# Optimization experiments

Measured on AMD Instinct MI355X. Metric: run time of the kernel, lower is better.

## Reference

```python
import jax, jax.numpy as jnp
import numpy as np

DIM = 512
HIDDEN = DIM * 4


def _act_quant(x):
    # per-token int8 absmax quant over last axis (BitNet b1.58)
    scale = 127.0 / jnp.clip(jnp.max(jnp.abs(x), axis=-1, keepdims=True), 1e-5)
    return jnp.clip(jnp.round(x * scale), -128.0, 127.0) / scale


def _weight_quant(w):
    # ternary {-1,0,1} quant with global mean-abs scale
    scale = 1.0 / jnp.clip(jnp.mean(jnp.abs(w)), 1e-5)
    return jnp.clip(jnp.round(w * scale), -1.0, 1.0) / scale


def _bitlinear(x, w, b):
    # straight-through estimator: forward uses quantized values
    xq = x + jax.lax.stop_gradient(_act_quant(x) - x)
    wq = w + jax.lax.stop_gradient(_weight_quant(w) - w)
    return jnp.einsum('btd,hd->bth', xq, wq) + b


def setup_inputs() -> dict:
    key = jax.random.key(0)
    k1, k2, k3 = jax.random.split(key, 3)
    x = jax.random.normal(k1, (8, 8192, DIM), dtype=jnp.float32)
    w1 = jax.random.normal(k2, (HIDDEN, DIM), dtype=jnp.float32) * (DIM ** -0.5)
    b1 = jnp.zeros((HIDDEN,), dtype=jnp.float32)
    w2 = jax.random.normal(k3, (DIM, HIDDEN), dtype=jnp.float32) * (HIDDEN ** -0.5)
    b2 = jnp.zeros((DIM,), dtype=jnp.float32)
    return {"x": x, "w1": w1, "b1": b1, "w2": w2, "b2": b2}


def reference(x, w1, b1, w2, b2):
    h = _bitlinear(x, w1, b1)                      # [B,T,HIDDEN]
    h = jax.nn.gelu(h, approximate=False)          # exact erf GELU (nn.GELU default)
    return x + _bitlinear(h, w2, b2)               # residual
```

## Files before the change

kernel.cpp:

```cpp
#include <hip/hip_runtime.h>
#include <hip/hip_bf16.h>

#define DIM 512
#define HID 2048
#define MT  64
#define KS1 8
#define KS2 32

typedef __attribute__((ext_vector_type(4))) int      i32x4;
typedef __attribute__((ext_vector_type(4))) unsigned u32x4;
typedef __attribute__((ext_vector_type(2))) unsigned u32x2;
typedef __attribute__((ext_vector_type(2))) __fp16   fp16x2;

#define ASET(ag, v) asm volatile("v_accvgpr_write_b32 %0, %1" : "=a"(ag) : "v"(v))
#define AGET(v, ag) asm volatile("v_accvgpr_read_b32 %0, %1" : "=v"(v) : "a"(ag))

static __device__ __forceinline__ float gelu_erf(float h) {
  const float u  = h * 0.70710678118654752f;
  const float au = fabsf(u);
  const float t  = __builtin_amdgcn_rcpf(fmaf(0.3275911f, au, 1.f));
  float p = fmaf(1.061405429f, t, -1.453152027f);
  p = fmaf(p, t, 1.421413741f);
  p = fmaf(p, t, -0.284496736f);
  p = fmaf(p, t, 0.254829592f);
  p *= t;
  const float e  = __builtin_amdgcn_exp2f(-u * u * 1.4426950408889634f);
  const float ea = fmaf(-p, e, 1.f);
  const float er = __builtin_copysignf(ea, u);
  return fmaf(0.5f * h, er, 0.5f * h);
}

static __device__ __forceinline__ int qi8(float g, float s) {
  return (int)fminf(fmaxf(rintf(g * s), -128.f), 127.f);
}

static __device__ __forceinline__ unsigned q4pack(float4 v, float scl) {
  int q0 = qi8(v.x, scl), q1 = qi8(v.y, scl), q2 = qi8(v.z, scl), q3 = qi8(v.w, scl);
  return (unsigned)(q0 & 255) | ((unsigned)(q1 & 255) << 8) |
         ((unsigned)(q2 & 255) << 16) | ((unsigned)(q3 & 255) << 24);
}

static __device__ __forceinline__ unsigned packf16(float a, float b) {
  fp16x2 v = __builtin_amdgcn_cvt_pkrtz(a, b);
  unsigned u; __builtin_memcpy(&u, &v, 4); return u;
}
static __device__ __forceinline__ float unpackf16(unsigned u, int hi) {
  unsigned short s = (unsigned short)(hi ? (u >> 16) : (u & 0xffff));
  __fp16 h; __builtin_memcpy(&h, &s, 2);
  return (float)h;
}

__global__ void k_wabs(const float* __restrict__ w1, const float* __restrict__ w2,
                       float* __restrict__ part) {
  const int b = blockIdx.x;
  const float* src = (b < 256 ? w1 : w2) + (size_t)(b & 255) * 4096 + threadIdx.x * 16;
  float s = 0.f;
#pragma unroll
  for (int i = 0; i < 4; ++i) {
    float4 v = *(const float4*)(src + i * 4);
    s += fabsf(v.x) + fabsf(v.y) + fabsf(v.z) + fabsf(v.w);
  }
  __shared__ float red[256];
  red[threadIdx.x] = s;
  __syncthreads();
  for (int off = 128; off > 0; off >>= 1) {
    if (threadIdx.x < (unsigned)off) red[threadIdx.x] += red[threadIdx.x + off];
    __syncthreads();
  }
  if (threadIdx.x == 0) part[b] = red[0];
}

__global__ void k_pack(const float* __restrict__ w1, const float* __restrict__ w2,
                       const float* __restrict__ part, float* __restrict__ scales,
                       signed char* __restrict__ p1, signed char* __restrict__ p2) {
  __shared__ float s1[256], s2[256];
  s1[threadIdx.x] = part[threadIdx.x];
  s2[threadIdx.x] = part[256 + threadIdx.x];
  __syncthreads();
  for (int off = 128; off > 0; off >>= 1) {
    if (threadIdx.x < (unsigned)off) {
      s1[threadIdx.x] += s1[threadIdx.x + off];
      s2[threadIdx.x] += s2[threadIdx.x + off];
    }
    __syncthreads();
  }
  const float mc1 = fmaxf(s1[0] / 1048576.f, 1e-5f);
  const float mc2 = fmaxf(s2[0] / 1048576.f, 1e-5f);
  if (blockIdx.x == 0 && threadIdx.x == 0) {
    scales[0] = mc1;
    scales[2] = mc2;
  }

  int slot = blockIdx.x * 256 + threadIdx.x;
  const bool isw2 = slot >= 65536;
  const float* w = isw2 ? w2 : w1;
  const float scl = 1.f / (isw2 ? mc2 : mc1);
  signed char* p = isw2 ? p2 : p1;
  const int K  = isw2 ? HID : DIM;
  const int KS = isw2 ? KS2 : KS1;
  slot &= 65535;
  const int lane = slot & 63;
  const int fr   = slot >> 6;
  const int nt   = fr / KS;
  const int ks   = fr - nt * KS;
  const int n  = nt * 16 + (lane & 15);
  const int k0 = ks * 64 + (lane >> 4) * 16;
  const float* src = w + (size_t)n * K + k0;
  i32x4 outv;
#pragma unroll
  for (int d = 0; d < 4; ++d) {
    unsigned v = 0;
#pragma unroll
    for (int e = 0; e < 4; ++e) {
      int q = (int)fminf(fmaxf(rintf(src[d * 4 + e] * scl), -1.f), 1.f);
      v |= ((unsigned)(q & 255)) << (8 * e);
    }
    outv[d] = (int)v;
  }
  *(i32x4*)(p + (size_t)slot * 16) = outv;
}

__global__ __launch_bounds__(1024, 4) void k_fused(
    const float* __restrict__ x, const float* __restrict__ b1,
    const float* __restrict__ b2, const signed char* __restrict__ p1,
    const signed char* __restrict__ p2, const float* __restrict__ scales,
    float* __restrict__ out) {
  __shared__ __align__(16) signed char qh[131072];
  __shared__ __align__(16) signed char xq[32768];

  float* rxTab = (float*)qh;
  float* scrP  = (float*)xq;
  float* scrS  = (float*)(xq + 8192);

  const int tid = threadIdx.x;
  const int wv = tid >> 6, ln = tid & 63, lg = ln >> 4, lr = ln & 15;
  const int tok0 = blockIdx.x * MT;
  const float wsc1 = scales[0], wsc2 = scales[2];
  const int swz = (lr & 7) << 4;

  {
    const int row = tid >> 4, sub = tid & 15;
    const float4* xr = (const float4*)(x + (size_t)(tok0 + row) * DIM);
    float4 v[8];
    float am = 0.f;
#pragma unroll
    for (int i = 0; i < 8; ++i) {
      v[i] = xr[i * 16 + sub];
      am = fmaxf(am, fmaxf(fmaxf(fabsf(v[i].x), fabsf(v[i].y)),
                           fmaxf(fabsf(v[i].z), fabsf(v[i].w))));
    }
#pragma unroll
    for (int m = 1; m < 16; m <<= 1) am = fmaxf(am, __shfl_xor(am, m));
    const float mc  = fmaxf(am, 1e-5f);
    const float scl = 127.f / mc;
    if (sub == 0) rxTab[row] = mc * (1.f / 127.f) * wsc1;
    const int rswz = (row & 7) << 4;
#pragma unroll
    for (int i = 0; i < 8; ++i) {
      const unsigned u = q4pack(v[i], scl);
      const int k = i * 64 + sub * 4;
      *(unsigned*)&xq[row * DIM + (((k & ~15) ^ rswz) | (k & 15))] = u;
    }
  }
  __syncthreads();

  float rxw[4];
#pragma unroll
  for (int mt = 0; mt < 4; ++mt) rxw[mt] = rxTab[mt * 16 + lr];
  __syncthreads();

  unsigned hvB[4][4][2];
  float hvmax[4], hvmin[4];
#pragma unroll
  for (int mt = 0; mt < 4; ++mt) { hvmax[mt] = -3.4e38f; hvmin[mt] = 3.4e38f; }

#define G1CHUNK(CH)                                                               \
  {                                                                               \
    i32x4 acc[4];                                                                 \
    _Pragma("unroll")                                                             \
    for (int mt = 0; mt < 4; ++mt) acc[mt] = (i32x4){0, 0, 0, 0};                 \
    const int ntg = (CH) * 16 + wv;                                               \
    _Pragma("unroll 2")                                                           \
    for (int ks = 0; ks < KS1; ++ks) {                                            \
      const i32x4 bfr =                                                           \
          *(const i32x4*)(p1 + ((size_t)(ntg * KS1 + ks) * 64 + ln) * 16);        \
      _Pragma("unroll")                                                           \
      for (int mt = 0; mt < 4; ++mt) {                                            \
        const i32x4 a = *(const i32x4*)&xq[(mt * 16 + lr) * DIM +                 \
                                           ((ks * 64 + lg * 16) ^ swz)];          \
        acc[mt] = __builtin_amdgcn_mfma_i32_16x16x64_i8(bfr, a, acc[mt],          \
                                                        0, 0, 0);                 \
      }                                                                           \
    }                                                                             \
    const float4 b4 = *(const float4*)&b1[ntg * 16 + lg * 4];                     \
    _Pragma("unroll")                                                             \
    for (int mt = 0; mt < 4; ++mt) {                                              \
      float hv[4];                                                                \
      _Pragma("unroll")                                                           \
      for (int r = 0; r < 4; ++r) {                                               \
        const float bias = r == 0 ? b4.x : r == 1 ? b4.y : r == 2 ? b4.z : b4.w;  \
        hv[r] = fmaf((float)acc[mt][r], rxw[mt], bias);                           \
        hvmax[mt] = fmaxf(hvmax[mt], hv[r]);                                      \
        hvmin[mt] = fminf(hvmin[mt], hv[r]);                                      \
      }                                                                           \
      const unsigned p0 = packf16(hv[0], hv[1]);                                  \
      const unsigned p1v = packf16(hv[2], hv[3]);                                 \
      if ((CH) < 4) {                                                             \
        const int row = mt * 16 + lr;                                             \
        const int bc  = ntg * 32 + lg * 8;        \
        u32x2 w2v; w2v[0] = p0; w2v[1] = p1v;                                     \
        *(u32x2*)&qh[row * 2048 + (((bc & ~15) ^ ((row & 7) << 4)) | (bc & 15))]  \
            = w2v;                                                                \
      } else {                                                                    \
        ASET(hvB[(CH) - 4][mt][0], p0);                                           \
        ASET(hvB[(CH) - 4][mt][1], p1v);                                          \
      }                                                                           \
    }                                                                             \
  }

  G1CHUNK(0)
  G1CHUNK(1)
  G1CHUNK(2)
  G1CHUNK(3)
  G1CHUNK(4)
  G1CHUNK(5)
  G1CHUNK(6)
  G1CHUNK(7)
#undef G1CHUNK
  __syncthreads();

#pragma unroll
  for (int mt = 0; mt < 4; ++mt) {
    hvmax[mt] = fmaxf(hvmax[mt], __shfl_xor(hvmax[mt], 16));
    hvmax[mt] = fmaxf(hvmax[mt], __shfl_xor(hvmax[mt], 32));
    hvmin[mt] = fminf(hvmin[mt], __shfl_xor(hvmin[mt], 16));
    hvmin[mt] = fminf(hvmin[mt], __shfl_xor(hvmin[mt], 32));
  }
  if (ln < 16) {
#pragma unroll
    for (int mt = 0; mt < 4; ++mt) {
      scrP[wv * 64 + mt * 16 + lr] = hvmax[mt];
      scrP[1024 + wv * 64 + mt * 16 + lr] = hvmin[mt];
    }
  }
  __syncthreads();
  if (tid < MT) {
    float hx = scrP[tid], hn = scrP[1024 + tid];
#pragma unroll
    for (int w = 1; w < 16; ++w) {
      hx = fmaxf(hx, scrP[w * 64 + tid]);
      hn = fminf(hn, scrP[1024 + w * 64 + tid]);
    }
    const float posg = gelu_erf(hx);
    const float negg = (hn <= -0.7518f) ? 0.1699705f : fabsf(gelu_erf(hn));
    scrS[tid] = 127.f / fmaxf(fmaxf(posg, negg), 1e-5f);
  }
  __syncthreads();

  float s2w[4], s2q[4];
#pragma unroll
  for (int mt = 0; mt < 4; ++mt) s2w[mt] = scrS[mt * 16 + lr];
#pragma unroll
  for (int k = 0; k < 4; ++k) s2q[k] = scrS[k * 16 + wv];
  __syncthreads();

#pragma unroll
  for (int k = 0; k < 4; ++k) {
    {
      const int rq  = k * 16 + wv;
      const int rsw = (rq & 7) << 4;
      const float sA = s2q[k];
      const u32x4 blk0 = *(const u32x4*)&qh[rq * 2048 + ((ln * 32) ^ rsw)];
      const u32x4 blk1 = *(const u32x4*)&qh[rq * 2048 + ((ln * 32 + 16) ^ rsw)];
      u32x4 o;
#pragma unroll
      for (int d = 0; d < 2; ++d) {
        const u32x4& blk = d ? blk1 : blk0;
#pragma unroll
        for (int e = 0; e < 2; ++e) {
          unsigned w = 0;
#pragma unroll
          for (int q = 0; q < 2; ++q) {
            const unsigned pv = blk[e * 2 + q];
            const int q0 = qi8(gelu_erf(unpackf16(pv, 0)), sA);
            const int q1 = qi8(gelu_erf(unpackf16(pv, 1)), sA);
            w |= ((unsigned)(q0 & 255)) << (16 * q);
            w |= ((unsigned)(q1 & 255)) << (16 * q + 8);
          }
          o[d * 2 + e] = w;
        }
      }
      signed char* dst = (rq < 16) ? (xq + rq * 2048) : (qh + (rq - 16) * 2048);
      *(u32x4*)&dst[(ln * 16) ^ rsw] = o;
    }
#pragma unroll
    for (int ch = 0; ch < 4; ++ch) {
      const int ntg = (ch + 4) * 16 + wv;
      const int m = k * 16 + lr;
      unsigned pk = 0;
#pragma unroll
      for (int pr = 0; pr < 2; ++pr) {
        unsigned v;
        AGET(v, hvB[ch][k][pr]);
        const int q0 = qi8(gelu_erf(unpackf16(v, 0)), s2w[k]);
        const int q1 = qi8(gelu_erf(unpackf16(v, 1)), s2w[k]);
        pk |= ((unsigned)(q0 & 255)) << (16 * pr);
        pk |= ((unsigned)(q1 & 255)) << (16 * pr + 8);
      }
      signed char* dst = (m < 16) ? (xq + m * 2048) : (qh + (m - 16) * 2048);
      *(unsigned*)&dst[(((ntg * 16) ^ ((m & 7) << 4)) + lg * 4)] = pk;
    }
    __syncthreads();
  }

  i32x4 acc2[2][4];
#pragma unroll
  for (int t = 0; t < 2; ++t)
#pragma unroll
    for (int mt = 0; mt < 4; ++mt) acc2[t][mt] = (i32x4){0, 0, 0, 0};
#pragma unroll 2
  for (int ks = 0; ks < KS2; ++ks) {
    i32x4 a[4];
    a[0] = *(const i32x4*)&xq[lr * 2048 + ((ks * 64 + lg * 16) ^ swz)];
#pragma unroll
    for (int mt = 1; mt < 4; ++mt)
      a[mt] = *(const i32x4*)&qh[((mt - 1) * 16 + lr) * 2048 +
                                 ((ks * 64 + lg * 16) ^ swz)];
#pragma unroll
    for (int t = 0; t < 2; ++t) {
      const int nt = wv * 2 + t;
      const i32x4 bfr = *(const i32x4*)(p2 + ((size_t)(nt * KS2 + ks) * 64 + ln) * 16);
#pragma unroll
      for (int mt = 0; mt < 4; ++mt)
        acc2[t][mt] = __builtin_amdgcn_mfma_i32_16x16x64_i8(bfr, a[mt], acc2[t][mt], 0, 0, 0);
    }
  }
#pragma unroll
  for (int t = 0; t < 2; ++t) {
    const int n0 = (wv * 2 + t) * 16 + lg * 4;
    const float4 b4 = *(const float4*)&b2[n0];
#pragma unroll
    for (int mt = 0; mt < 4; ++mt) {
      const int m = mt * 16 + lr;
      const float r2 = wsc2 * __builtin_amdgcn_rcpf(s2w[mt]);
      const size_t gbase = (size_t)(tok0 + m) * DIM + n0;
      const float4 x4 = *(const float4*)&x[gbase];
      float4 o;
      o.x = fmaf((float)acc2[t][mt][0], r2, b4.x + x4.x);
      o.y = fmaf((float)acc2[t][mt][1], r2, b4.y + x4.y);
      o.z = fmaf((float)acc2[t][mt][2], r2, b4.z + x4.z);
      o.w = fmaf((float)acc2[t][mt][3], r2, b4.w + x4.w);
      *(float4*)&out[gbase] = o;
    }
  }
}

extern "C" void kernel_launch(void* const* d_in, const int* in_sizes, int n_in,
                              void* d_out, int out_size, void* d_ws, size_t ws_size,
                              hipStream_t stream) {
  const float* x  = (const float*)d_in[0];
  const float* w1 = (const float*)d_in[1];
  const float* b1 = (const float*)d_in[2];
  const float* w2 = (const float*)d_in[3];
  const float* b2 = (const float*)d_in[4];
  float* out = (float*)d_out;

  float* wpart   = (float*)d_ws;
  float* wscales = wpart + 512;
  signed char* p1 = (signed char*)((char*)d_ws + 4096);
  signed char* p2 = (signed char*)((char*)d_ws + 4096 + 1048576);

  k_wabs<<<512, 256, 0, stream>>>(w1, w2, wpart);
  k_pack<<<512, 256, 0, stream>>>(w1, w2, wpart, wscales, p1, p2);
  k_fused<<<1024, 1024, 0, stream>>>(x, b1, b2, p1, p2, wscales, out);
}
```

Measured before the change: 343.4 us.

## Quantize hidden activations in place within qh, removing per-chunk barriers

Instead of staggering the GELU+int8 requantization over four passes with a barrier each and spilling rows into the xq buffer, each row of packed fp16 hidden values is now converted in place inside the same LDS region. It does the first half, the shared-memory portion, in one pass, then the accumulator-held portion, then synchronizes once. The second GEMM reads all A fragments from a single buffer. This cuts the barrier count and the cross-buffer addressing. The risk is in-place overwrite hazards: each row is read and written by the same wave with a compacted layout, so correctness depends on the index mapping.

```diff
diff --git a/kernel.cpp b/kernel.cpp
--- a/kernel.cpp
+++ b/kernel.cpp
@@ -48,6 +48,11 @@
   unsigned short s = (unsigned short)(hi ? (u >> 16) : (u & 0xffff));
   __fp16 h; __builtin_memcpy(&h, &s, 2);
   return (float)h;
+}
+static __device__ __forceinline__ unsigned q2f16(unsigned pv, float s) {
+  const int q0 = qi8(gelu_erf(unpackf16(pv, 0)), s);
+  const int q1 = qi8(gelu_erf(unpackf16(pv, 1)), s);
+  return (unsigned)(q0 & 255) | ((unsigned)(q1 & 255) << 8);
 }
 
 __global__ void k_wabs(const float* __restrict__ w1, const float* __restrict__ w2,
@@ -257,61 +262,44 @@
   }
   __syncthreads();
 
-  float s2w[4], s2q[4];
+  float s2w[4];
 #pragma unroll
   for (int mt = 0; mt < 4; ++mt) s2w[mt] = scrS[mt * 16 + lr];
-#pragma unroll
-  for (int k = 0; k < 4; ++k) s2q[k] = scrS[k * 16 + wv];
-  __syncthreads();
-
-#pragma unroll
-  for (int k = 0; k < 4; ++k) {
-    {
-      const int rq  = k * 16 + wv;
-      const int rsw = (rq & 7) << 4;
-      const float sA = s2q[k];
-      const u32x4 blk0 = *(const u32x4*)&qh[rq * 2048 + ((ln * 32) ^ rsw)];
-      const u32x4 blk1 = *(const u32x4*)&qh[rq * 2048 + ((ln * 32 + 16) ^ rsw)];
-      u32x4 o;
-#pragma unroll
-      for (int d = 0; d < 2; ++d) {
-        const u32x4& blk = d ? blk1 : blk0;
-#pragma unroll
-        for (int e = 0; e < 2; ++e) {
-          unsigned w = 0;
-#pragma unroll
-          for (int q = 0; q < 2; ++q) {
-            const unsigned pv = blk[e * 2 + q];
-            const int q0 = qi8(gelu_erf(unpackf16(pv, 0)), sA);
-            const int q1 = qi8(gelu_erf(unpackf16(pv, 1)), sA);
-            w |= ((unsigned)(q0 & 255)) << (16 * q);
-            w |= ((unsigned)(q1 & 255)) << (16 * q + 8);
-          }
-          o[d * 2 + e] = w;
-        }
-      }
-      signed char* dst = (rq < 16) ? (xq + rq * 2048) : (qh + (rq - 16) * 2048);
-      *(u32x4*)&dst[(ln * 16) ^ rsw] = o;
-    }
-#pragma unroll
-    for (int ch = 0; ch < 4; ++ch) {
+
+#pragma unroll
+  for (int i = 0; i < 4; ++i) {
+    const int rq  = wv + 16 * i;
+    const int rsw = (rq & 7) << 4;
+    const float sA = scrS[rq];
+    const u32x4 blkA = *(const u32x4*)&qh[rq * 2048 + ((16 * ln) ^ rsw)];
+    const u32x4 blkB = *(const u32x4*)&qh[rq * 2048 + 1024 + ((16 * ln) ^ rsw)];
+    unsigned oa0 = q2f16(blkA[0], sA) | (q2f16(blkA[1], sA) << 16);
+    unsigned oa1 = q2f16(blkA[2], sA) | (q2f16(blkA[3], sA) << 16);
+    unsigned ob0 = q2f16(blkB[0], sA) | (q2f16(blkB[1], sA) << 16);
+    unsigned ob1 = q2f16(blkB[2], sA) | (q2f16(blkB[3], sA) << 16);
+    const int c0 = 8 * ln;
+    const int c1 = 512 + 8 * ln;
+    u32x2 wa; wa[0] = oa0; wa[1] = oa1;
+    u32x2 wb; wb[0] = ob0; wb[1] = ob1;
+    *(u32x2*)&qh[rq * 2048 + (((c0 & ~15) ^ rsw) | (c0 & 15))] = wa;
+    *(u32x2*)&qh[rq * 2048 + (((c1 & ~15) ^ rsw) | (c1 & 15))] = wb;
+  }
+  __syncthreads();
+
+#pragma unroll
+  for (int ch = 0; ch < 4; ++ch) {
+#pragma unroll
+    for (int mt = 0; mt < 4; ++mt) {
       const int ntg = (ch + 4) * 16 + wv;
-      const int m = k * 16 + lr;
-      unsigned pk = 0;
-#pragma unroll
-      for (int pr = 0; pr < 2; ++pr) {
-        unsigned v;
-        AGET(v, hvB[ch][k][pr]);
-        const int q0 = qi8(gelu_erf(unpackf16(v, 0)), s2w[k]);
-        const int q1 = qi8(gelu_erf(unpackf16(v, 1)), s2w[k]);
-        pk |= ((unsigned)(q0 & 255)) << (16 * pr);
-        pk |= ((unsigned)(q1 & 255)) << (16 * pr + 8);
-      }
-      signed char* dst = (m < 16) ? (xq + m * 2048) : (qh + (m - 16) * 2048);
-      *(unsigned*)&dst[(((ntg * 16) ^ ((m & 7) << 4)) + lg * 4)] = pk;
-    }
-    __syncthreads();
-  }
+      const int m = mt * 16 + lr;
+      unsigned v0, v1;
+      AGET(v0, hvB[ch][mt][0]);
+      AGET(v1, hvB[ch][mt][1]);
+      const unsigned pk = q2f16(v0, s2w[mt]) | (q2f16(v1, s2w[mt]) << 16);
+      *(unsigned*)&qh[m * 2048 + (((ntg * 16) ^ ((m & 7) << 4)) + lg * 4)] = pk;
+    }
+  }
+  __syncthreads();
 
   i32x4 acc2[2][4];
 #pragma unroll
@@ -321,11 +309,9 @@
 #pragma unroll 2
   for (int ks = 0; ks < KS2; ++ks) {
     i32x4 a[4];
-    a[0] = *(const i32x4*)&xq[lr * 2048 + ((ks * 64 + lg * 16) ^ swz)];
-#pragma unroll
-    for (int mt = 1; mt < 4; ++mt)
-      a[mt] = *(const i32x4*)&qh[((mt - 1) * 16 + lr) * 2048 +
-                                 ((ks * 64 + lg * 16) ^ swz)];
+#pragma unroll
+    for (int mt = 0; mt < 4; ++mt)
+      a[mt] = *(const i32x4*)&qh[(mt * 16 + lr) * 2048 + ((ks * 64 + lg * 16) ^ swz)];
 #pragma unroll
     for (int t = 0; t < 2; ++t) {
       const int nt = wv * 2 + t;
```

Result: slower. 356.9 us (+3.9%).
